# Optimization experiments

Hardware: AMD Instinct MI355X
Metric: run time of the kernel (lower is better)

The kernel has to match this reference:

```python
import jax, jax.numpy as jnp
import numpy as np

B, T, C, H = 8, 2048, 1024, 128  # batch, seq (== block_size), embed dim, head size


def setup_inputs() -> dict:
    key = jax.random.key(0)
    kx, kq, kk, kv = jax.random.split(key, 4)
    x = jax.random.normal(kx, (B, T, C), dtype=jnp.float32)
    # torch Linear(no bias) weights: [head_size, in_features], applied as x @ W.T
    s = 1.0 / np.sqrt(C)
    Wq = jax.random.normal(kq, (H, C), dtype=jnp.float32) * s
    Wk = jax.random.normal(kk, (H, C), dtype=jnp.float32) * s
    Wv = jax.random.normal(kv, (H, C), dtype=jnp.float32) * s
    return {"x": x, "Wq": Wq, "Wk": Wk, "Wv": Wv}


def reference(x, Wq, Wk, Wv):
    # projections: [B,T,C] @ [C,H] -> [B,T,H]
    q = jnp.einsum('btc,hc->bth', x, Wq)
    k = jnp.einsum('btc,hc->bth', x, Wk)
    v = jnp.einsum('btc,hc->bth', x, Wv)
    scale = k.shape[-1] ** -0.5
    # scores [B,T,T], causal mask, softmax in fp32 (autocast disabled in original)
    scores = jnp.einsum('bqh,bkh->bqk', q, k) * scale
    causal = jnp.tril(jnp.ones((T, T), dtype=bool))
    scores = jnp.where(causal, scores, -jnp.inf)
    attn = jax.nn.softmax(scores.astype(jnp.float32), axis=-1)
    # dropout_rate = 0.0 -> identity
    out = jnp.einsum('bqk,bkh->bqh', attn.astype(v.dtype), v)
    return out
```

## Files before the change

### kernel.cpp

```cpp
#include <hip/hip_runtime.h>
#include <hip/hip_bf16.h>

constexpr int NB = 8;
constexpr int T  = 2048;
constexpr int C  = 1024;
constexpr int Hd = 128;

typedef short bf16x8 __attribute__((ext_vector_type(8)));
typedef float floatx4 __attribute__((ext_vector_type(4)));

__device__ __forceinline__ ushort f2bf(float x) {
    return __builtin_bit_cast(ushort, __float2bfloat16(x));
}
__device__ __forceinline__ float bf2f(ushort u) {
    unsigned int x = ((unsigned int)u) << 16;
    return __builtin_bit_cast(float, x);
}
__device__ __forceinline__ void async16(ushort* lds, const ushort* g) {
    __builtin_amdgcn_global_load_lds(
        (const __attribute__((address_space(1))) unsigned int*)g,
        (__attribute__((address_space(3))) unsigned int*)lds, 16, 0, 0);
}

__global__ __launch_bounds__(256) void convert_xw(
    const float* __restrict__ X, const float* __restrict__ Wq,
    const float* __restrict__ Wk, const float* __restrict__ Wv,
    ushort* __restrict__ Xb, ushort* __restrict__ Wb)
{
    int bid = blockIdx.x;
    if (bid < 8192) {
        size_t i = ((size_t)bid * 256 + threadIdx.x) * 8;
        float4 a = *(const float4*)&X[i];
        float4 b = *(const float4*)&X[i + 4];
        bf16x8 o;
        o[0] = (short)f2bf(a.x); o[1] = (short)f2bf(a.y);
        o[2] = (short)f2bf(a.z); o[3] = (short)f2bf(a.w);
        o[4] = (short)f2bf(b.x); o[5] = (short)f2bf(b.y);
        o[6] = (short)f2bf(b.z); o[7] = (short)f2bf(b.w);
        *(bf16x8*)&Xb[i] = o;
    } else {
        int g = (bid - 8192) * 256 + threadIdx.x;
        size_t base = (size_t)g * 8;
        int sel = (int)(base >> 17);
        const float* W = sel == 0 ? Wq : (sel == 1 ? Wk : Wv);
        float s = (sel == 0) ? 0.12751744f : 1.0f;
        size_t off = base - (size_t)sel * 131072;
        float4 a = *(const float4*)&W[off];
        float4 b = *(const float4*)&W[off + 4];
        bf16x8 o;
        o[0] = (short)f2bf(a.x * s); o[1] = (short)f2bf(a.y * s);
        o[2] = (short)f2bf(a.z * s); o[3] = (short)f2bf(a.w * s);
        o[4] = (short)f2bf(b.x * s); o[5] = (short)f2bf(b.y * s);
        o[6] = (short)f2bf(b.z * s); o[7] = (short)f2bf(b.w * s);
        *(bf16x8*)&Wb[base] = o;
    }
}

__global__ __launch_bounds__(256) void qkv_gemm(
    const ushort* __restrict__ Xb, const ushort* __restrict__ Wb,
    ushort* __restrict__ Qo, ushort* __restrict__ Ko, ushort* __restrict__ Vt)
{
    __shared__ ushort SM[12288];
    ushort* Al = SM;
    ushort* Bl = SM + 8192;
    const int m0 = blockIdx.x * 128;
    const int n0 = blockIdx.y * 64;
    const int tid = threadIdx.x, lane = tid & 63, wave = tid >> 6;
    const int quad = lane >> 4, colL = lane & 15;
    const int wm = (wave & 1) * 64, wn = (wave >> 1) * 32;
    const int lr = lane >> 3;
    const int lcs = ((lane & 7) ^ (lr & 7)) * 8;

    floatx4 acc[4][2] = {};

    for (int k0 = 0; k0 < C; k0 += 64) {
        for (int t = 0; t < 4; ++t) {
            int q = wave * 4 + t;
            async16(&Al[q * 512 + lane * 8],
                    &Xb[(size_t)(m0 + q * 8 + lr) * C + k0 + lcs]);
        }
        for (int t = 0; t < 2; ++t) {
            int q = wave * 2 + t;
            async16(&Bl[q * 512 + lane * 8],
                    &Wb[(size_t)(n0 + q * 8 + lr) * C + k0 + lcs]);
        }
        __syncthreads();

        bf16x8 af[2][4], bfr[2][2];
        for (int kk = 0; kk < 2; ++kk) {
            for (int mt = 0; mt < 4; ++mt)
                af[kk][mt] = *(const bf16x8*)
                    &Al[(wm + mt * 16 + colL) * 64 + (((kk * 4 + quad) ^ (colL & 7))) * 8];
            for (int nt = 0; nt < 2; ++nt)
                bfr[kk][nt] = *(const bf16x8*)
                    &Bl[(wn + nt * 16 + colL) * 64 + (((kk * 4 + quad) ^ (colL & 7))) * 8];
        }
        for (int kk = 0; kk < 2; ++kk)
            for (int mt = 0; mt < 4; ++mt)
                for (int nt = 0; nt < 2; ++nt)
                    acc[mt][nt] = __builtin_amdgcn_mfma_f32_16x16x32_bf16(
                        af[kk][mt], bfr[kk][nt], acc[mt][nt], 0, 0, 0);
        __syncthreads();
    }

    const int sel = n0 >> 7;
    const int h0 = n0 & 127;
    if (sel < 2) {
        ushort* dst = sel == 0 ? Qo : Ko;
        for (int mt = 0; mt < 4; ++mt)
            for (int nt = 0; nt < 2; ++nt)
                for (int r = 0; r < 4; ++r) {
                    int row = m0 + wm + mt * 16 + quad * 4 + r;
                    int h = h0 + wn + nt * 16 + colL;
                    dst[(size_t)row * Hd + h] = f2bf(acc[mt][nt][r]);
                }
    } else {
        ushort* TL = SM;
        for (int mt = 0; mt < 4; ++mt)
            for (int nt = 0; nt < 2; ++nt)
                for (int r = 0; r < 4; ++r)
                    TL[(wm + mt * 16 + quad * 4 + r) * 66 + wn + nt * 16 + colL] =
                        f2bf(acc[mt][nt][r]);
        __syncthreads();
        const int b = m0 >> 11, tb = m0 & 2047;
        const int h = tid & 63, tq = tid >> 6;
        for (int st = 0; st < 4; ++st) {
            int t0 = tq * 32 + st * 8;
            bf16x8 o;
            for (int jx = 0; jx < 8; ++jx)
                o[jx] = (short)TL[(t0 + jx) * 66 + h];
            *(bf16x8*)&Vt[((size_t)b * Hd + h0 + h) * T + tb + t0] = o;
        }
    }
}

__global__ __launch_bounds__(256, 2) void attn_partial(
    const ushort* __restrict__ Q, const ushort* __restrict__ Kg,
    const ushort* __restrict__ Vt, ushort* __restrict__ Opart,
    float* __restrict__ mpart, float* __restrict__ lpart)
{
    __shared__ ushort Kl[128 * 128];
    __shared__ ushort Vl[128 * 128];

    const int tid = threadIdx.x, lane = tid & 63, wave = tid >> 6;
    const int quad = lane >> 4, colL = lane & 15;

    int id = blockIdx.x;
    int b = id / 136;
    int rem = id - b * 136;
    int j = 15;
    while (rem >= j + 1) { rem -= (j + 1); --j; }
    int c = rem;
    const int q0 = j * 128;
    const int k0 = c * 128;
    const bool diag = (c == j);

    {
        int r = tid >> 4, p = tid & 15;
        for (int t = 0; t < 8; ++t) {
            int row = t * 16 + r;
            async16(&Kl[t * 2048 + tid * 8],
                    &Kg[((size_t)b * T + k0 + row) * Hd + ((p ^ (row & 15)) * 8)]);
        }
        for (int t = 0; t < 8; ++t) {
            int hrow = t * 16 + r;
            async16(&Vl[t * 2048 + tid * 8],
                    &Vt[((size_t)b * Hd + hrow) * T + k0 + ((p ^ (hrow & 15)) * 8)]);
        }
    }

    bf16x8 qa[2][4];
    for (int mi = 0; mi < 2; ++mi) {
        const ushort* qp =
            &Q[((size_t)b * T + q0 + wave * 32 + mi * 16 + colL) * Hd + quad * 8];
        for (int ks = 0; ks < 4; ++ks)
            qa[mi][ks] = *(const bf16x8*)&qp[ks * 32];
    }

    __syncthreads();

    floatx4 accS[2][8] = {};
    for (int ks = 0; ks < 4; ++ks)
        for (int nt = 0; nt < 8; ++nt) {
            int krow = nt * 16 + colL;
            bf16x8 kb = *(const bf16x8*)&Kl[krow * 128 + (((ks * 4 + quad) ^ colL) * 8)];
            accS[0][nt] = __builtin_amdgcn_mfma_f32_16x16x32_bf16(qa[0][ks], kb, accS[0][nt], 0, 0, 0);
            accS[1][nt] = __builtin_amdgcn_mfma_f32_16x16x32_bf16(qa[1][ks], kb, accS[1][nt], 0, 0, 0);
        }

    if (diag) {
        for (int mi = 0; mi < 2; ++mi)
            for (int nt = 0; nt < 8; ++nt)
                for (int rr = 0; rr < 4; ++rr) {
                    int lrow = wave * 32 + mi * 16 + quad * 4 + rr;
                    int lcol = nt * 16 + colL;
                    if (lcol > lrow) accS[mi][nt][rr] = -__builtin_inff();
                }
    }
    __syncthreads();

    ushort* Pw = &Kl[wave * 4096];
    float m_r[2][4], l_r[2][4];
    for (int mi = 0; mi < 2; ++mi)
        for (int rr = 0; rr < 4; ++rr) {
            float mx = accS[mi][0][rr];
            for (int nt = 1; nt < 8; ++nt) mx = fmaxf(mx, accS[mi][nt][rr]);
            for (int off = 1; off < 16; off <<= 1)
                mx = fmaxf(mx, __shfl_xor(mx, off, 64));
            m_r[mi][rr] = mx;
            l_r[mi][rr] = 0.f;
        }
    for (int mi = 0; mi < 2; ++mi) {
        for (int nt = 0; nt < 8; ++nt)
            for (int rr = 0; rr < 4; ++rr) {
                float p = __builtin_amdgcn_exp2f(accS[mi][nt][rr] - m_r[mi][rr]);
                l_r[mi][rr] += p;
                int prow = mi * 16 + quad * 4 + rr;
                Pw[prow * 128 + ((nt * 16 + colL) ^ ((prow & 7) << 4))] = f2bf(p);
            }
        for (int rr = 0; rr < 4; ++rr) {
            float s = l_r[mi][rr];
            for (int off = 1; off < 16; off <<= 1)
                s += __shfl_xor(s, off, 64);
            l_r[mi][rr] = s;
        }
    }

    bf16x8 pa[2][4];
    for (int mi = 0; mi < 2; ++mi) {
        int prow = mi * 16 + colL;
        int sw = (prow & 7) << 4;
        for (int ks = 0; ks < 4; ++ks)
            pa[mi][ks] = *(const bf16x8*)&Pw[prow * 128 + ((ks * 32 + quad * 8) ^ sw)];
    }

    floatx4 Oacc[2][8] = {};
    for (int ks = 0; ks < 4; ++ks)
        for (int th = 0; th < 8; ++th) {
            int hrow = th * 16 + colL;
            bf16x8 vb = *(const bf16x8*)&Vl[hrow * 128 + (((ks * 4 + quad) ^ colL) * 8)];
            Oacc[0][th] = __builtin_amdgcn_mfma_f32_16x16x32_bf16(pa[0][ks], vb, Oacc[0][th], 0, 0, 0);
            Oacc[1][th] = __builtin_amdgcn_mfma_f32_16x16x32_bf16(pa[1][ks], vb, Oacc[1][th], 0, 0, 0);
        }

    const int slot = b * 136 + (j * (j + 1)) / 2 + c;
    ushort* Op = &Opart[(size_t)slot * 16384];
    for (int mi = 0; mi < 2; ++mi)
        for (int th = 0; th < 8; ++th)
            for (int rr = 0; rr < 4; ++rr) {
                int row = wave * 32 + mi * 16 + quad * 4 + rr;
                Op[row * 128 + th * 16 + colL] = f2bf(Oacc[mi][th][rr]);
            }
    if (colL == 0)
        for (int mi = 0; mi < 2; ++mi)
            for (int rr = 0; rr < 4; ++rr) {
                int row = wave * 32 + mi * 16 + quad * 4 + rr;
                mpart[(size_t)slot * 128 + row] = m_r[mi][rr];
                lpart[(size_t)slot * 128 + row] = l_r[mi][rr];
            }
}

__global__ __launch_bounds__(256) void attn_combine(
    const ushort* __restrict__ Opart, const float* __restrict__ mpart,
    const float* __restrict__ lpart, float* __restrict__ out)
{
    const int j = blockIdx.x, b = blockIdx.y;
    const int nch = j + 1;
    const int sbase = b * 136 + (j * (j + 1)) / 2;
    const int t = threadIdx.x;
    const int row = blockIdx.z * 32 + (t >> 3);
    const int h0 = (t & 7) * 16;

    float M = -__builtin_inff();
    for (int c = 0; c < nch; ++c)
        M = fmaxf(M, mpart[(size_t)(sbase + c) * 128 + row]);
    float ltot = 0.f;
    for (int c = 0; c < nch; ++c)
        ltot += lpart[(size_t)(sbase + c) * 128 + row] *
                __builtin_amdgcn_exp2f(mpart[(size_t)(sbase + c) * 128 + row] - M);

    float o[16];
    for (int i = 0; i < 16; ++i) o[i] = 0.f;
    for (int c = 0; c < nch; ++c) {
        float wgt = __builtin_amdgcn_exp2f(mpart[(size_t)(sbase + c) * 128 + row] - M);
        const ushort* Op = &Opart[(size_t)(sbase + c) * 16384 + row * 128 + h0];
        for (int x = 0; x < 2; ++x) {
            bf16x8 v = *(const bf16x8*)&Op[x * 8];
            for (int i2 = 0; i2 < 8; ++i2)
                o[x * 8 + i2] += bf2f((ushort)v[i2]) * wgt;
        }
    }
    float inv = 1.0f / ltot;
    float* dst = &out[((size_t)(b * T) + j * 128 + row) * Hd + h0];
    for (int i = 0; i < 16; ++i) dst[i] = o[i] * inv;
}

extern "C" void kernel_launch(void* const* d_in, const int* in_sizes, int n_in,
                              void* d_out, int out_size, void* d_ws, size_t ws_size,
                              hipStream_t stream) {
    const float* x  = (const float*)d_in[0];
    const float* Wq = (const float*)d_in[1];
    const float* Wk = (const float*)d_in[2];
    const float* Wv = (const float*)d_in[3];
    float* out = (float*)d_out;

    char* w = (char*)d_ws;
    ushort* Xb = (ushort*)w;
    ushort* Wb = (ushort*)(w + (size_t)33554432);
    ushort* Opart = (ushort*)w;
    float* mpart = (float*)(w + (size_t)35651584);
    float* lpart = (float*)(w + (size_t)35651584 + 557056);
    w += (size_t)35651584 + 2 * 557056;
    ushort* Qb  = (ushort*)w;  w += (size_t)NB * T * Hd * 2;
    ushort* Kb  = (ushort*)w;  w += (size_t)NB * T * Hd * 2;
    ushort* Vtb = (ushort*)w;  w += (size_t)NB * T * Hd * 2;

    convert_xw<<<8384, 256, 0, stream>>>(x, Wq, Wk, Wv, Xb, Wb);
    qkv_gemm<<<dim3(128, 6), 256, 0, stream>>>(Xb, Wb, Qb, Kb, Vtb);
    attn_partial<<<1088, 256, 0, stream>>>(Qb, Kb, Vtb, Opart, mpart, lpart);
    attn_combine<<<dim3(16, 8, 4), 256, 0, stream>>>(Opart, mpart, lpart, out);
}
```

Baseline: 164.0 us.

## Process two key chunks per attention block with online softmax rescaling

Each attn_partial block now walks two consecutive 128-key chunks with an online-softmax rescale of its running max, sum and output accumulator. This halves the number of partial outputs and the grid size (1088 to 576 blocks), and so cuts Opart/m/l writes and the combine kernel's reads. Batch index is now the fastest-varying part of the block id. The combine kernel is unrolled over up to 8 chunks with m/l values cached in registers. The cost is fewer blocks for the GPU to spread across its compute units and a serial second K/V load with no prefetch overlap.

```diff
diff --git a/kernel.cpp b/kernel.cpp
--- a/kernel.cpp
+++ b/kernel.cpp
@@ -146,17 +146,17 @@
     const int quad = lane >> 4, colL = lane & 15;
 
     int id = blockIdx.x;
-    int b = id / 136;
-    int rem = id - b * 136;
+    int b = id & 7;
+    int rem = id >> 3;
     int j = 15;
-    while (rem >= j + 1) { rem -= (j + 1); --j; }
-    int c = rem;
+    while (rem >= (j >> 1) + 1) { rem -= (j >> 1) + 1; --j; }
+    const int c = rem;
     const int q0 = j * 128;
-    const int k0 = c * 128;
-    const bool diag = (c == j);
+    const int nchunk = (2 * c + 1 <= j) ? 2 : 1;
 
     {
-        int r = tid >> 4, p = tid & 15;
+        const int k0 = 2 * c * 128;
+        const int r = tid >> 4, p = tid & 15;
         for (int t = 0; t < 8; ++t) {
             int row = t * 16 + r;
             async16(&Kl[t * 2048 + tid * 8],
@@ -177,73 +177,118 @@
             qa[mi][ks] = *(const bf16x8*)&qp[ks * 32];
     }
 
-    __syncthreads();
-
-    floatx4 accS[2][8] = {};
-    for (int ks = 0; ks < 4; ++ks)
-        for (int nt = 0; nt < 8; ++nt) {
-            int krow = nt * 16 + colL;
-            bf16x8 kb = *(const bf16x8*)&Kl[krow * 128 + (((ks * 4 + quad) ^ colL) * 8)];
-            accS[0][nt] = __builtin_amdgcn_mfma_f32_16x16x32_bf16(qa[0][ks], kb, accS[0][nt], 0, 0, 0);
-            accS[1][nt] = __builtin_amdgcn_mfma_f32_16x16x32_bf16(qa[1][ks], kb, accS[1][nt], 0, 0, 0);
-        }
-
-    if (diag) {
-        for (int mi = 0; mi < 2; ++mi)
-            for (int nt = 0; nt < 8; ++nt)
-                for (int rr = 0; rr < 4; ++rr) {
-                    int lrow = wave * 32 + mi * 16 + quad * 4 + rr;
-                    int lcol = nt * 16 + colL;
-                    if (lcol > lrow) accS[mi][nt][rr] = -__builtin_inff();
-                }
-    }
-    __syncthreads();
-
-    ushort* Pw = &Kl[wave * 4096];
+    floatx4 Oacc[2][8] = {};
     float m_r[2][4], l_r[2][4];
     for (int mi = 0; mi < 2; ++mi)
         for (int rr = 0; rr < 4; ++rr) {
-            float mx = accS[mi][0][rr];
-            for (int nt = 1; nt < 8; ++nt) mx = fmaxf(mx, accS[mi][nt][rr]);
-            for (int off = 1; off < 16; off <<= 1)
-                mx = fmaxf(mx, __shfl_xor(mx, off, 64));
-            m_r[mi][rr] = mx;
+            m_r[mi][rr] = -__builtin_inff();
             l_r[mi][rr] = 0.f;
         }
-    for (int mi = 0; mi < 2; ++mi) {
-        for (int nt = 0; nt < 8; ++nt)
+
+    for (int kk = 0; kk < nchunk; ++kk) {
+        const int chunk = 2 * c + kk;
+        const bool diag = (chunk == j);
+
+        if (kk > 0) {
+            __syncthreads();
+            const int k0 = chunk * 128;
+            const int r = tid >> 4, p = tid & 15;
+            for (int t = 0; t < 8; ++t) {
+                int row = t * 16 + r;
+                async16(&Kl[t * 2048 + tid * 8],
+                        &Kg[((size_t)b * T + k0 + row) * Hd + ((p ^ (row & 15)) * 8)]);
+            }
+            for (int t = 0; t < 8; ++t) {
+                int hrow = t * 16 + r;
+                async16(&Vl[t * 2048 + tid * 8],
+                        &Vt[((size_t)b * Hd + hrow) * T + k0 + ((p ^ (hrow & 15)) * 8)]);
+            }
+        }
+        __syncthreads();
+
+        floatx4 accS[2][8] = {};
+        for (int ks = 0; ks < 4; ++ks)
+            for (int nt = 0; nt < 8; ++nt) {
+                int krow = nt * 16 + colL;
+                bf16x8 kb = *(const bf16x8*)&Kl[krow * 128 + (((ks * 4 + quad) ^ colL) * 8)];
+                accS[0][nt] = __builtin_amdgcn_mfma_f32_16x16x32_bf16(qa[0][ks], kb, accS[0][nt], 0, 0, 0);
+                accS[1][nt] = __builtin_amdgcn_mfma_f32_16x16x32_bf16(qa[1][ks], kb, accS[1][nt], 0, 0, 0);
+            }
+
+        if (diag) {
+            for (int mi = 0; mi < 2; ++mi)
+                for (int nt = 0; nt < 8; ++nt)
+                    for (int rr = 0; rr < 4; ++rr) {
+                        int lrow = wave * 32 + mi * 16 + quad * 4 + rr;
+                        int lcol = nt * 16 + colL;
+                        if (lcol > lrow) accS[mi][nt][rr] = -__builtin_inff();
+                    }
+        }
+        __syncthreads();
+
+        float sc[2][4];
+        for (int mi = 0; mi < 2; ++mi)
             for (int rr = 0; rr < 4; ++rr) {
-                float p = __builtin_amdgcn_exp2f(accS[mi][nt][rr] - m_r[mi][rr]);
-                l_r[mi][rr] += p;
-                int prow = mi * 16 + quad * 4 + rr;
-                Pw[prow * 128 + ((nt * 16 + colL) ^ ((prow & 7) << 4))] = f2bf(p);
-            }
-        for (int rr = 0; rr < 4; ++rr) {
-            float s = l_r[mi][rr];
-            for (int off = 1; off < 16; off <<= 1)
-                s += __shfl_xor(s, off, 64);
-            l_r[mi][rr] = s;
-        }
-    }
-
-    bf16x8 pa[2][4];
-    for (int mi = 0; mi < 2; ++mi) {
-        int prow = mi * 16 + colL;
-        int sw = (prow & 7) << 4;
+                float mx = accS[mi][0][rr];
+                for (int nt = 1; nt < 8; ++nt) mx = fmaxf(mx, accS[mi][nt][rr]);
+                for (int off = 1; off < 16; off <<= 1)
+                    mx = fmaxf(mx, __shfl_xor(mx, off, 64));
+                if (kk == 0) {
+                    m_r[mi][rr] = mx;
+                    sc[mi][rr] = 1.0f;
+                } else {
+                    float nm = fmaxf(m_r[mi][rr], mx);
+                    sc[mi][rr] = __builtin_amdgcn_exp2f(m_r[mi][rr] - nm);
+                    m_r[mi][rr] = nm;
+                }
+            }
+        if (kk > 0) {
+            for (int mi = 0; mi < 2; ++mi)
+                for (int rr = 0; rr < 4; ++rr)
+                    l_r[mi][rr] *= sc[mi][rr];
+            for (int mi = 0; mi < 2; ++mi)
+                for (int th = 0; th < 8; ++th)
+                    for (int rr = 0; rr < 4; ++rr)
+                        Oacc[mi][th][rr] *= sc[mi][rr];
+        }
+
+        ushort* Pw = &Kl[wave * 4096];
+        for (int mi = 0; mi < 2; ++mi) {
+            float ls[4] = {0.f, 0.f, 0.f, 0.f};
+            for (int nt = 0; nt < 8; ++nt)
+                for (int rr = 0; rr < 4; ++rr) {
+                    float p = __builtin_amdgcn_exp2f(accS[mi][nt][rr] - m_r[mi][rr]);
+                    ls[rr] += p;
+                    int prow = mi * 16 + quad * 4 + rr;
+                    Pw[prow * 128 + ((nt * 16 + colL) ^ ((prow & 7) << 4))] = f2bf(p);
+                }
+            for (int rr = 0; rr < 4; ++rr) {
+                float s = ls[rr];
+                for (int off = 1; off < 16; off <<= 1)
+                    s += __shfl_xor(s, off, 64);
+                l_r[mi][rr] += s;
+            }
+        }
+
+        bf16x8 pa[2][4];
+        for (int mi = 0; mi < 2; ++mi) {
+            int prow = mi * 16 + colL;
+            int sw = (prow & 7) << 4;
+            for (int ks = 0; ks < 4; ++ks)
+                pa[mi][ks] = *(const bf16x8*)&Pw[prow * 128 + ((ks * 32 + quad * 8) ^ sw)];
+        }
+
         for (int ks = 0; ks < 4; ++ks)
-            pa[mi][ks] = *(const bf16x8*)&Pw[prow * 128 + ((ks * 32 + quad * 8) ^ sw)];
-    }
-
-    floatx4 Oacc[2][8] = {};
-    for (int ks = 0; ks < 4; ++ks)
-        for (int th = 0; th < 8; ++th) {
-            int hrow = th * 16 + colL;
-            bf16x8 vb = *(const bf16x8*)&Vl[hrow * 128 + (((ks * 4 + quad) ^ colL) * 8)];
-            Oacc[0][th] = __builtin_amdgcn_mfma_f32_16x16x32_bf16(pa[0][ks], vb, Oacc[0][th], 0, 0, 0);
-            Oacc[1][th] = __builtin_amdgcn_mfma_f32_16x16x32_bf16(pa[1][ks], vb, Oacc[1][th], 0, 0, 0);
-        }
-
-    const int slot = b * 136 + (j * (j + 1)) / 2 + c;
+            for (int th = 0; th < 8; ++th) {
+                int hrow = th * 16 + colL;
+                bf16x8 vb = *(const bf16x8*)&Vl[hrow * 128 + (((ks * 4 + quad) ^ colL) * 8)];
+                Oacc[0][th] = __builtin_amdgcn_mfma_f32_16x16x32_bf16(pa[0][ks], vb, Oacc[0][th], 0, 0, 0);
+                Oacc[1][th] = __builtin_amdgcn_mfma_f32_16x16x32_bf16(pa[1][ks], vb, Oacc[1][th], 0, 0, 0);
+            }
+    }
+
+    const int hj = j >> 1;
+    const int slot = b * 72 + hj * hj + hj + (j & 1) * (hj + 1) + c;
     ushort* Op = &Opart[(size_t)slot * 16384];
     for (int mi = 0; mi < 2; ++mi)
         for (int th = 0; th < 8; ++th)
@@ -265,29 +310,44 @@
     const float* __restrict__ lpart, float* __restrict__ out)
 {
     const int j = blockIdx.x, b = blockIdx.y;
-    const int nch = j + 1;
-    const int sbase = b * 136 + (j * (j + 1)) / 2;
+    const int nch = (j >> 1) + 1;
+    const int hj = j >> 1;
+    const int sbase = b * 72 + hj * hj + hj + (j & 1) * (hj + 1);
     const int t = threadIdx.x;
     const int row = blockIdx.z * 32 + (t >> 3);
     const int h0 = (t & 7) * 16;
 
+    float mv[8], lv[8], wgt[8];
     float M = -__builtin_inff();
-    for (int c = 0; c < nch; ++c)
-        M = fmaxf(M, mpart[(size_t)(sbase + c) * 128 + row]);
+#pragma unroll
+    for (int cc = 0; cc < 8; ++cc) {
+        if (cc < nch) {
+            mv[cc] = mpart[(size_t)(sbase + cc) * 128 + row];
+            lv[cc] = lpart[(size_t)(sbase + cc) * 128 + row];
+            M = fmaxf(M, mv[cc]);
+        }
+    }
     float ltot = 0.f;
-    for (int c = 0; c < nch; ++c)
-        ltot += lpart[(size_t)(sbase + c) * 128 + row] *
-                __builtin_amdgcn_exp2f(mpart[(size_t)(sbase + c) * 128 + row] - M);
+#pragma unroll
+    for (int cc = 0; cc < 8; ++cc) {
+        if (cc < nch) {
+            wgt[cc] = __builtin_amdgcn_exp2f(mv[cc] - M);
+            ltot += lv[cc] * wgt[cc];
+        }
+    }
 
     float o[16];
+#pragma unroll
     for (int i = 0; i < 16; ++i) o[i] = 0.f;
-    for (int c = 0; c < nch; ++c) {
-        float wgt = __builtin_amdgcn_exp2f(mpart[(size_t)(sbase + c) * 128 + row] - M);
-        const ushort* Op = &Opart[(size_t)(sbase + c) * 16384 + row * 128 + h0];
-        for (int x = 0; x < 2; ++x) {
-            bf16x8 v = *(const bf16x8*)&Op[x * 8];
-            for (int i2 = 0; i2 < 8; ++i2)
-                o[x * 8 + i2] += bf2f((ushort)v[i2]) * wgt;
+#pragma unroll
+    for (int cc = 0; cc < 8; ++cc) {
+        if (cc < nch) {
+            const ushort* Op = &Opart[(size_t)(sbase + cc) * 16384 + row * 128 + h0];
+            for (int x = 0; x < 2; ++x) {
+                bf16x8 v = *(const bf16x8*)&Op[x * 8];
+                for (int i2 = 0; i2 < 8; ++i2)
+                    o[x * 8 + i2] += bf2f((ushort)v[i2]) * wgt[cc];
+            }
         }
     }
     float inv = 1.0f / ltot;
@@ -317,6 +377,6 @@
 
     convert_xw<<<8384, 256, 0, stream>>>(x, Wq, Wk, Wv, Xb, Wb);
     qkv_gemm<<<dim3(128, 6), 256, 0, stream>>>(Xb, Wb, Qb, Kb, Vtb);
-    attn_partial<<<1088, 256, 0, stream>>>(Qb, Kb, Vtb, Opart, mpart, lpart);
+    attn_partial<<<576, 256, 0, stream>>>(Qb, Kb, Vtb, Opart, mpart, lpart);
     attn_combine<<<dim3(16, 8, 4), 256, 0, stream>>>(Opart, mpart, lpart, out);
 }
```

New measurement: 200.5 us. 1.22x slower.
